# Optimization experiments

Hardware: AMD Instinct MI355X
Metric: run time of the kernel (lower is better)

Reference implementation:

```python
import jax, jax.numpy as jnp
import numpy as np
from jax import lax

N_ITERS = 128  # fixed iteration budget for geodesic reconstruction (image is 256x256;
# true convergence is data-dependent; 128 sweeps of 3x3 dilation covers typical propagation)

NEG_INF = -1e30


def _dilate3x3(x):
    # grayscale dilation with a 3x3 flat structuring element, NHWC
    return lax.reduce_window(x, NEG_INF, lax.max,
                             window_dimensions=(1, 3, 3, 1),
                             window_strides=(1, 1, 1, 1),
                             padding='SAME')


def h_maxima(img, h):
    # reconstruction by dilation of (img - h) under img
    mask = img
    marker = img - h

    def step(m, _):
        m = jnp.minimum(_dilate3x3(m), mask)
        return m, None

    marker, _ = lax.scan(step, marker, None, length=N_ITERS)
    return marker


def setup_inputs() -> dict:
    key = jax.random.key(0)
    k1, k2 = jax.random.split(key)
    B, H, W, C = 128, 256, 256, 1
    img = jax.random.uniform(k1, (B, H, W, C), dtype=jnp.float32)
    # h in (0, 0.3): typical contrast threshold for h-maxima on [0,1] images
    h = jax.random.uniform(k2, (B, 1, 1, 1), dtype=jnp.float32) * 0.3
    return {"img": img, "h": h}


def reference(img, h):
    return h_maxima(img, h)
```

## Files before the change

kernel.cpp:

```cpp
#include <hip/hip_runtime.h>
#include <stdint.h>


#define NEGPAIR 0xFBFFFBFFu
#define TITER 128
#define GROUPS 64

typedef _Float16 h2  __attribute__((ext_vector_type(2)));
typedef __fp16   fh2 __attribute__((ext_vector_type(2)));

static __device__ __forceinline__ uint32_t pmax(uint32_t a, uint32_t b) {
    uint32_t r;
    asm("v_pk_max_f16 %0, %1, %2" : "=v"(r) : "v"(a), "v"(b));
    return r;
}
static __device__ __forceinline__ uint32_t pmin(uint32_t a, uint32_t b) {
    uint32_t r;
    asm("v_pk_min_f16 %0, %1, %2" : "=v"(r) : "v"(a), "v"(b));
    return r;
}
static __device__ __forceinline__ uint32_t alignb(uint32_t hi, uint32_t lo) {
    return __builtin_amdgcn_alignbit(hi, lo, 16);
}
static __device__ __forceinline__ uint32_t pack2(float lo, float hi) {
    fh2 p = __builtin_amdgcn_cvt_pkrtz(lo, hi);
    return __builtin_bit_cast(uint32_t, p);
}
static __device__ __forceinline__ uint32_t dpp_shr1(uint32_t s) {
    return (uint32_t)__builtin_amdgcn_update_dpp((int)NEGPAIR, (int)s, 0x111, 0xF, 0xF, false);
}
static __device__ __forceinline__ uint32_t dpp_shl1(uint32_t s) {
    return (uint32_t)__builtin_amdgcn_update_dpp((int)NEGPAIR, (int)s, 0x101, 0xF, 0xF, false);
}

struct W8 { uint32_t s0, s1, s2, s3, s4, s5, s6, s7; };

static __device__ __forceinline__ W8 ld8(const uint32_t* p) {
    uint4 a = reinterpret_cast<const uint4*>(p)[0];
    uint4 b = reinterpret_cast<const uint4*>(p)[1];
    W8 w;
    w.s0 = a.x; w.s1 = a.y; w.s2 = a.z; w.s3 = a.w;
    w.s4 = b.x; w.s5 = b.y; w.s6 = b.z; w.s7 = b.w;
    return w;
}
static __device__ __forceinline__ void st8(uint32_t* p, W8 w) {
    reinterpret_cast<uint4*>(p)[0] = make_uint4(w.s0, w.s1, w.s2, w.s3);
    reinterpret_cast<uint4*>(p)[1] = make_uint4(w.s4, w.s5, w.s6, w.s7);
}
static __device__ __forceinline__ W8 wmax(W8 a, W8 b) {
    W8 r;
    r.s0 = pmax(a.s0, b.s0); r.s1 = pmax(a.s1, b.s1);
    r.s2 = pmax(a.s2, b.s2); r.s3 = pmax(a.s3, b.s3);
    r.s4 = pmax(a.s4, b.s4); r.s5 = pmax(a.s5, b.s5);
    r.s6 = pmax(a.s6, b.s6); r.s7 = pmax(a.s7, b.s7);
    return r;
}
static __device__ __forceinline__ W8 wneg() {
    W8 r;
    r.s0 = NEGPAIR; r.s1 = NEGPAIR; r.s2 = NEGPAIR; r.s3 = NEGPAIR;
    r.s4 = NEGPAIR; r.s5 = NEGPAIR; r.s6 = NEGPAIR; r.s7 = NEGPAIR;
    return r;
}
static __device__ __forceinline__ uint32_t wdiff(W8 a, W8 b) {
    return (a.s0 ^ b.s0) | (a.s1 ^ b.s1) | (a.s2 ^ b.s2) | (a.s3 ^ b.s3) |
           (a.s4 ^ b.s4) | (a.s5 ^ b.s5) | (a.s6 ^ b.s6) | (a.s7 ^ b.s7);
}

static __device__ __forceinline__ W8 hpass(W8 v, W8 k) {
    uint32_t lv = dpp_shr1(v.s7);
    uint32_t rv = dpp_shl1(v.s0);
    W8 m;
    m.s0 = pmin(pmax(pmax(v.s0, alignb(v.s0, lv)),   alignb(v.s1, v.s0)), k.s0);
    m.s1 = pmin(pmax(pmax(v.s1, alignb(v.s1, v.s0)), alignb(v.s2, v.s1)), k.s1);
    m.s2 = pmin(pmax(pmax(v.s2, alignb(v.s2, v.s1)), alignb(v.s3, v.s2)), k.s2);
    m.s3 = pmin(pmax(pmax(v.s3, alignb(v.s3, v.s2)), alignb(v.s4, v.s3)), k.s3);
    m.s4 = pmin(pmax(pmax(v.s4, alignb(v.s4, v.s3)), alignb(v.s5, v.s4)), k.s4);
    m.s5 = pmin(pmax(pmax(v.s5, alignb(v.s5, v.s4)), alignb(v.s6, v.s5)), k.s5);
    m.s6 = pmin(pmax(pmax(v.s6, alignb(v.s6, v.s5)), alignb(v.s7, v.s6)), k.s6);
    m.s7 = pmin(pmax(pmax(v.s7, alignb(v.s7, v.s6)), alignb(rv,   v.s7)), k.s7);
    return m;
}

__global__ __launch_bounds__(1024, 1) void hx_full(
    const float* __restrict__ img,
    const float* __restrict__ hh,
    float*       __restrict__ fout)
{
    __shared__ uint32_t A[2][GROUPS][128];
    __shared__ uint32_t B[2][GROUPS][128];

    const int tid = threadIdx.x;
    const int seg = tid & 15;
    const int g   = tid >> 4;
    const int b   = blockIdx.x;
    const int sw  = seg * 8;

    uint32_t* f0p = &B[0][0][0];
    uint32_t* f1p = &B[1][0][0];
    uint32_t* f2p = &A[0][GROUPS - 1][0];
    uint32_t* cg0 = &A[0][GROUPS - 1][8];
    uint32_t* cg1 = &A[1][GROUPS - 1][8];
    if (tid == 0) { *f0p = 0; *f1p = 0; *f2p = 0; }
    if (tid < 66) {
        uint32_t v = (tid >= 1 && tid <= 64) ? 1u : 0u;
        cg0[tid] = v; cg1[tid] = v;
    }
    uint32_t *pW = f0p, *pR = f2p, *pZ = f1p;

    W8 m0, m1, m2, m3, k0, k1, k2, k3;
    const float hb = hh[b];
    {
        const size_t ib = ((size_t)b << 16) + ((size_t)(4 * g) << 8) + seg * 16;
        #pragma unroll
        for (int r = 0; r < 4; ++r) {
            const float4* src = reinterpret_cast<const float4*>(img + ib + ((size_t)r << 8));
            float4 fa = src[0], fb = src[1], fc = src[2], fd = src[3];
            W8 kv, mv;
            kv.s0 = pack2(fa.x, fa.y);       kv.s1 = pack2(fa.z, fa.w);
            kv.s2 = pack2(fb.x, fb.y);       kv.s3 = pack2(fb.z, fb.w);
            kv.s4 = pack2(fc.x, fc.y);       kv.s5 = pack2(fc.z, fc.w);
            kv.s6 = pack2(fd.x, fd.y);       kv.s7 = pack2(fd.z, fd.w);
            mv.s0 = pack2(fa.x-hb, fa.y-hb); mv.s1 = pack2(fa.z-hb, fa.w-hb);
            mv.s2 = pack2(fb.x-hb, fb.y-hb); mv.s3 = pack2(fb.z-hb, fb.w-hb);
            mv.s4 = pack2(fc.x-hb, fc.y-hb); mv.s5 = pack2(fc.z-hb, fc.w-hb);
            mv.s6 = pack2(fd.x-hb, fd.y-hb); mv.s7 = pack2(fd.z-hb, fd.w-hb);
            if (r == 0) { m0 = mv; k0 = kv; }
            else if (r == 1) { m1 = mv; k1 = kv; }
            else if (r == 2) { m2 = mv; k2 = kv; }
            else { m3 = mv; k3 = kv; }
        }
    }

    for (int t = 0; t < TITER; ++t) {
        const int p = t & 1;
        if (g < GROUPS - 1) st8(&A[p][g][sw], m3);
        if (g > 0)          st8(&B[p][g][sw], m0);
        __syncthreads();
        const uint32_t* cgR = p ? cg0 : cg1;
        uint32_t*       cgW = p ? cg1 : cg0;
        uint32_t fexit = *pR;
        uint32_t act   = cgR[g] | cgR[g + 1] | cgR[g + 2];
        if (t > 0 && fexit == 0) break;
        uint32_t cbit;
        if (__any(act != 0)) {
            W8 ab = (g > 0)          ? ld8(&A[p][g - 1][sw]) : wneg();
            W8 bl = (g < GROUPS - 1) ? ld8(&B[p][g + 1][sw]) : wneg();
            W8 t01 = wmax(m0, m1);
            W8 t12 = wmax(m1, m2);
            W8 t23 = wmax(m2, m3);
            W8 nm1 = hpass(wmax(t01, m2), k1);
            W8 nm2 = hpass(wmax(t12, m3), k2);
            W8 v0  = wmax(ab, t01);
            W8 v3  = wmax(t23, bl);
            W8 nm0 = hpass(v0, k0);
            W8 nm3 = hpass(v3, k3);
            uint32_t ch = wdiff(nm0, m0) | wdiff(nm1, m1) |
                          wdiff(nm2, m2) | wdiff(nm3, m3);
            uint32_t c = ch;
            c |= __shfl_xor(c, 1); c |= __shfl_xor(c, 2);
            c |= __shfl_xor(c, 4); c |= __shfl_xor(c, 8);
            cbit = c ? 1u : 0u;
            if (seg == 0) {
                cgW[g + 1] = cbit;
                if (cbit) *pW = 1;
            }
            m0 = nm0; m1 = nm1; m2 = nm2; m3 = nm3;
        } else {
            cbit = 0;
            if (seg == 0) cgW[g + 1] = 0;
        }
        if (tid == 0) *pZ = 0;
        uint32_t* tp = pW; pW = pZ; pZ = pR; pR = tp;
    }

    {
        const size_t ob = ((size_t)b << 16) + ((size_t)(4 * g) << 8) + seg * 16;
        #pragma unroll
        for (int r = 0; r < 4; ++r) {
            W8 mv = (r == 0) ? m0 : (r == 1) ? m1 : (r == 2) ? m2 : m3;
            float* orow = fout + ob + ((size_t)r << 8);
            h2 x, y; float4 f;
            x = __builtin_bit_cast(h2, mv.s0); y = __builtin_bit_cast(h2, mv.s1);
            f.x = (float)x.x; f.y = (float)x.y; f.z = (float)y.x; f.w = (float)y.y;
            reinterpret_cast<float4*>(orow)[0] = f;
            x = __builtin_bit_cast(h2, mv.s2); y = __builtin_bit_cast(h2, mv.s3);
            f.x = (float)x.x; f.y = (float)x.y; f.z = (float)y.x; f.w = (float)y.y;
            reinterpret_cast<float4*>(orow)[1] = f;
            x = __builtin_bit_cast(h2, mv.s4); y = __builtin_bit_cast(h2, mv.s5);
            f.x = (float)x.x; f.y = (float)x.y; f.z = (float)y.x; f.w = (float)y.y;
            reinterpret_cast<float4*>(orow)[2] = f;
            x = __builtin_bit_cast(h2, mv.s6); y = __builtin_bit_cast(h2, mv.s7);
            f.x = (float)x.x; f.y = (float)x.y; f.z = (float)y.x; f.w = (float)y.y;
            reinterpret_cast<float4*>(orow)[3] = f;
        }
    }
}

extern "C" void kernel_launch(void* const* d_in, const int* in_sizes, int n_in,
                              void* d_out, int out_size, void* d_ws, size_t ws_size,
                              hipStream_t stream) {
    const float* img = (const float*)d_in[0];
    const float* hh  = (const float*)d_in[1];
    hx_full<<<128, 1024, 0, stream>>>(img, hh, (float*)d_out);
}
```

Measured before the change: 123.4 us.

## Fuse two dilation sweeps per barrier with 8-row thread tiles and halo recompute

Each thread now holds 8 rows instead of 4, and the block shrinks to 512 threads. The loop runs 64 steps, and each step exchanges two boundary rows with each neighbour and performs two dilation-plus-clamp sweeps. The second sweep recomputes the halo rows from loaded neighbour rows and their mask rows. This halves the number of block barriers and convergence checks, in exchange for redundant halo compute and much more live register state. The launch bound of (512,2) may force register spilling, and it leaves each CU with half the threads.

```diff
diff --git a/kernel.cpp b/kernel.cpp
--- a/kernel.cpp
+++ b/kernel.cpp
@@ -3,8 +3,8 @@
 
 
 #define NEGPAIR 0xFBFFFBFFu
-#define TITER 128
-#define GROUPS 64
+#define STEPS 64
+#define GROUPS 32
 
 typedef _Float16 h2  __attribute__((ext_vector_type(2)));
 typedef __fp16   fh2 __attribute__((ext_vector_type(2)));
@@ -81,17 +81,29 @@
     return m;
 }
 
-__global__ __launch_bounds__(1024, 1) void hx_full(
+static __device__ __forceinline__ W8 ldrow_f32(const float* img, int b, int ir, int seg) {
+    const float4* src = reinterpret_cast<const float4*>(
+        img + ((size_t)b << 16) + ((size_t)ir << 8) + seg * 16);
+    float4 fa = src[0], fb = src[1], fc = src[2], fd = src[3];
+    W8 w;
+    w.s0 = pack2(fa.x, fa.y); w.s1 = pack2(fa.z, fa.w);
+    w.s2 = pack2(fb.x, fb.y); w.s3 = pack2(fb.z, fb.w);
+    w.s4 = pack2(fc.x, fc.y); w.s5 = pack2(fc.z, fc.w);
+    w.s6 = pack2(fd.x, fd.y); w.s7 = pack2(fd.z, fd.w);
+    return w;
+}
+
+__global__ __launch_bounds__(512, 2) void hx_full(
     const float* __restrict__ img,
     const float* __restrict__ hh,
     float*       __restrict__ fout)
 {
-    __shared__ uint32_t A[2][GROUPS][128];
-    __shared__ uint32_t B[2][GROUPS][128];
+    __shared__ uint32_t A[2][GROUPS][256];
+    __shared__ uint32_t B[2][GROUPS][256];
 
     const int tid = threadIdx.x;
     const int seg = tid & 15;
-    const int g   = tid >> 4;
+    const int G   = tid >> 4;
     const int b   = blockIdx.x;
     const int sw  = seg * 8;
 
@@ -101,83 +113,106 @@
     uint32_t* cg0 = &A[0][GROUPS - 1][8];
     uint32_t* cg1 = &A[1][GROUPS - 1][8];
     if (tid == 0) { *f0p = 0; *f1p = 0; *f2p = 0; }
-    if (tid < 66) {
-        uint32_t v = (tid >= 1 && tid <= 64) ? 1u : 0u;
+    if (tid < 34) {
+        uint32_t v = (tid >= 1 && tid <= 32) ? 1u : 0u;
         cg0[tid] = v; cg1[tid] = v;
     }
     uint32_t *pW = f0p, *pR = f2p, *pZ = f1p;
 
-    W8 m0, m1, m2, m3, k0, k1, k2, k3;
+    W8 m0,m1,m2,m3,m4,m5,m6,m7, k0,k1,k2,k3,k4,k5,k6,k7, ka,kb;
     const float hb = hh[b];
     {
-        const size_t ib = ((size_t)b << 16) + ((size_t)(4 * g) << 8) + seg * 16;
+        const int r0 = 8 * G;
+        k0 = ldrow_f32(img, b, r0+0, seg); k1 = ldrow_f32(img, b, r0+1, seg);
+        k2 = ldrow_f32(img, b, r0+2, seg); k3 = ldrow_f32(img, b, r0+3, seg);
+        k4 = ldrow_f32(img, b, r0+4, seg); k5 = ldrow_f32(img, b, r0+5, seg);
+        k6 = ldrow_f32(img, b, r0+6, seg); k7 = ldrow_f32(img, b, r0+7, seg);
+        ka = (G > 0)          ? ldrow_f32(img, b, r0 - 1, seg) : wneg();
+        kb = (G < GROUPS - 1) ? ldrow_f32(img, b, r0 + 8, seg) : wneg();
+        const uint32_t hp = pack2(hb, hb);
+        const float4* src = reinterpret_cast<const float4*>(
+            img + ((size_t)b << 16) + ((size_t)r0 << 8) + seg * 16);
+        (void)hp; (void)src;
         #pragma unroll
-        for (int r = 0; r < 4; ++r) {
-            const float4* src = reinterpret_cast<const float4*>(img + ib + ((size_t)r << 8));
-            float4 fa = src[0], fb = src[1], fc = src[2], fd = src[3];
-            W8 kv, mv;
-            kv.s0 = pack2(fa.x, fa.y);       kv.s1 = pack2(fa.z, fa.w);
-            kv.s2 = pack2(fb.x, fb.y);       kv.s3 = pack2(fb.z, fb.w);
-            kv.s4 = pack2(fc.x, fc.y);       kv.s5 = pack2(fc.z, fc.w);
-            kv.s6 = pack2(fd.x, fd.y);       kv.s7 = pack2(fd.z, fd.w);
-            mv.s0 = pack2(fa.x-hb, fa.y-hb); mv.s1 = pack2(fa.z-hb, fa.w-hb);
-            mv.s2 = pack2(fb.x-hb, fb.y-hb); mv.s3 = pack2(fb.z-hb, fb.w-hb);
-            mv.s4 = pack2(fc.x-hb, fc.y-hb); mv.s5 = pack2(fc.z-hb, fc.w-hb);
-            mv.s6 = pack2(fd.x-hb, fd.y-hb); mv.s7 = pack2(fd.z-hb, fd.w-hb);
-            if (r == 0) { m0 = mv; k0 = kv; }
-            else if (r == 1) { m1 = mv; k1 = kv; }
-            else if (r == 2) { m2 = mv; k2 = kv; }
-            else { m3 = mv; k3 = kv; }
+        for (int r = 0; r < 8; ++r) {
+            const float4* s2 = reinterpret_cast<const float4*>(
+                img + ((size_t)b << 16) + ((size_t)(r0 + r) << 8) + seg * 16);
+            float4 fa = s2[0], fb2 = s2[1], fc = s2[2], fd = s2[3];
+            W8 mv;
+            mv.s0 = pack2(fa.x-hb, fa.y-hb);  mv.s1 = pack2(fa.z-hb, fa.w-hb);
+            mv.s2 = pack2(fb2.x-hb, fb2.y-hb); mv.s3 = pack2(fb2.z-hb, fb2.w-hb);
+            mv.s4 = pack2(fc.x-hb, fc.y-hb);  mv.s5 = pack2(fc.z-hb, fc.w-hb);
+            mv.s6 = pack2(fd.x-hb, fd.y-hb);  mv.s7 = pack2(fd.z-hb, fd.w-hb);
+            if (r == 0) m0 = mv; else if (r == 1) m1 = mv;
+            else if (r == 2) m2 = mv; else if (r == 3) m3 = mv;
+            else if (r == 4) m4 = mv; else if (r == 5) m5 = mv;
+            else if (r == 6) m6 = mv; else m7 = mv;
         }
     }
 
-    for (int t = 0; t < TITER; ++t) {
-        const int p = t & 1;
-        if (g < GROUPS - 1) st8(&A[p][g][sw], m3);
-        if (g > 0)          st8(&B[p][g][sw], m0);
+    for (int s = 0; s < STEPS; ++s) {
+        const int p = s & 1;
+        if (G < GROUPS - 1) { st8(&A[p][G][sw], m6); st8(&A[p][G][128 + sw], m7); }
+        if (G > 0)          { st8(&B[p][G][sw], m0); st8(&B[p][G][128 + sw], m1); }
         __syncthreads();
         const uint32_t* cgR = p ? cg0 : cg1;
         uint32_t*       cgW = p ? cg1 : cg0;
         uint32_t fexit = *pR;
-        uint32_t act   = cgR[g] | cgR[g + 1] | cgR[g + 2];
-        if (t > 0 && fexit == 0) break;
+        uint32_t act   = cgR[G] | cgR[G + 1] | cgR[G + 2];
+        if (s > 0 && fexit == 0) break;
         uint32_t cbit;
         if (__any(act != 0)) {
-            W8 ab = (g > 0)          ? ld8(&A[p][g - 1][sw]) : wneg();
-            W8 bl = (g < GROUPS - 1) ? ld8(&B[p][g + 1][sw]) : wneg();
-            W8 t01 = wmax(m0, m1);
-            W8 t12 = wmax(m1, m2);
-            W8 t23 = wmax(m2, m3);
-            W8 nm1 = hpass(wmax(t01, m2), k1);
-            W8 nm2 = hpass(wmax(t12, m3), k2);
-            W8 v0  = wmax(ab, t01);
-            W8 v3  = wmax(t23, bl);
-            W8 nm0 = hpass(v0, k0);
-            W8 nm3 = hpass(v3, k3);
-            uint32_t ch = wdiff(nm0, m0) | wdiff(nm1, m1) |
-                          wdiff(nm2, m2) | wdiff(nm3, m3);
+            W8 ha0, ha1, hb0, hb1;
+            if (G > 0) { ha0 = ld8(&A[p][G-1][sw]); ha1 = ld8(&A[p][G-1][128+sw]); }
+            else       { ha0 = wneg(); ha1 = wneg(); }
+            if (G < GROUPS - 1) { hb0 = ld8(&B[p][G+1][sw]); hb1 = ld8(&B[p][G+1][128+sw]); }
+            else                { hb0 = wneg(); hb1 = wneg(); }
+            W8 qa = hpass(wmax(wmax(ha0, ha1), m0), ka);
+            W8 q0 = hpass(wmax(wmax(ha1, m0), m1), k0);
+            W8 q1 = hpass(wmax(wmax(m0, m1), m2), k1);
+            W8 q2 = hpass(wmax(wmax(m1, m2), m3), k2);
+            W8 q3 = hpass(wmax(wmax(m2, m3), m4), k3);
+            W8 q4 = hpass(wmax(wmax(m3, m4), m5), k4);
+            W8 q5 = hpass(wmax(wmax(m4, m5), m6), k5);
+            W8 q6 = hpass(wmax(wmax(m5, m6), m7), k6);
+            W8 q7 = hpass(wmax(wmax(m6, m7), hb0), k7);
+            W8 qb = hpass(wmax(wmax(m7, hb0), hb1), kb);
+            W8 n0 = hpass(wmax(wmax(qa, q0), q1), k0);
+            W8 n1 = hpass(wmax(wmax(q0, q1), q2), k1);
+            W8 n2 = hpass(wmax(wmax(q1, q2), q3), k2);
+            W8 n3 = hpass(wmax(wmax(q2, q3), q4), k3);
+            W8 n4 = hpass(wmax(wmax(q3, q4), q5), k4);
+            W8 n5 = hpass(wmax(wmax(q4, q5), q6), k5);
+            W8 n6 = hpass(wmax(wmax(q5, q6), q7), k6);
+            W8 n7 = hpass(wmax(wmax(q6, q7), qb), k7);
+            uint32_t ch = wdiff(n0, m0) | wdiff(n1, m1) | wdiff(n2, m2) |
+                          wdiff(n3, m3) | wdiff(n4, m4) | wdiff(n5, m5) |
+                          wdiff(n6, m6) | wdiff(n7, m7);
             uint32_t c = ch;
             c |= __shfl_xor(c, 1); c |= __shfl_xor(c, 2);
             c |= __shfl_xor(c, 4); c |= __shfl_xor(c, 8);
             cbit = c ? 1u : 0u;
             if (seg == 0) {
-                cgW[g + 1] = cbit;
+                cgW[G + 1] = cbit;
                 if (cbit) *pW = 1;
             }
-            m0 = nm0; m1 = nm1; m2 = nm2; m3 = nm3;
+            m0 = n0; m1 = n1; m2 = n2; m3 = n3;
+            m4 = n4; m5 = n5; m6 = n6; m7 = n7;
         } else {
             cbit = 0;
-            if (seg == 0) cgW[g + 1] = 0;
+            if (seg == 0) cgW[G + 1] = 0;
         }
         if (tid == 0) *pZ = 0;
         uint32_t* tp = pW; pW = pZ; pZ = pR; pR = tp;
     }
 
     {
-        const size_t ob = ((size_t)b << 16) + ((size_t)(4 * g) << 8) + seg * 16;
+        const size_t ob = ((size_t)b << 16) + ((size_t)(8 * G) << 8) + seg * 16;
         #pragma unroll
-        for (int r = 0; r < 4; ++r) {
-            W8 mv = (r == 0) ? m0 : (r == 1) ? m1 : (r == 2) ? m2 : m3;
+        for (int r = 0; r < 8; ++r) {
+            W8 mv = (r == 0) ? m0 : (r == 1) ? m1 : (r == 2) ? m2 :
+                    (r == 3) ? m3 : (r == 4) ? m4 : (r == 5) ? m5 :
+                    (r == 6) ? m6 : m7;
             float* orow = fout + ob + ((size_t)r << 8);
             h2 x, y; float4 f;
             x = __builtin_bit_cast(h2, mv.s0); y = __builtin_bit_cast(h2, mv.s1);
@@ -201,5 +236,5 @@
                               hipStream_t stream) {
     const float* img = (const float*)d_in[0];
     const float* hh  = (const float*)d_in[1];
-    hx_full<<<128, 1024, 0, stream>>>(img, hh, (float*)d_out);
-}
+    hx_full<<<128, 512, 0, stream>>>(img, hh, (float*)d_out);
+}
```

After: 139.9 us. 13.4% more time.
